# Performance work log

Hardware: AMD Instinct MI355X
Metric: run time of the kernel (lower is better)

Reference implementation:

```python
import jax, jax.numpy as jnp
import numpy as np

N = 100_000      # num nodes
E = 1_600_000    # num edges
F_IN = 128       # input feature dim
H = 128          # hidden dim
C = 16           # num classes
R = 5            # num relations


def setup_inputs() -> dict:
    key = jax.random.key(0)
    ks = jax.random.split(key, 12)
    x = jax.random.normal(ks[0], (N, F_IN), jnp.float32)
    edge_index = jax.random.randint(ks[1], (2, E), 0, N, dtype=jnp.int64)
    edge_weight = jax.random.uniform(ks[2], (E,), jnp.float32)
    edge_type = jax.random.randint(ks[3], (E,), 0, R, dtype=jnp.int64)
    # RGCNConv params (no basis decomposition): per-relation weight, root, bias
    s1 = 1.0 / np.sqrt(F_IN).astype(np.float32)
    s2 = 1.0 / np.sqrt(H).astype(np.float32)
    W1 = jax.random.normal(ks[4], (R, F_IN, H), jnp.float32) * s1
    root1 = jax.random.normal(ks[5], (F_IN, H), jnp.float32) * s1
    b1 = jnp.zeros((H,), jnp.float32)
    W2 = jax.random.normal(ks[6], (R, H, C), jnp.float32) * s2
    root2 = jax.random.normal(ks[7], (H, C), jnp.float32) * s2
    b2 = jnp.zeros((C,), jnp.float32)
    return {"x": x, "edge_index": edge_index, "edge_weight": edge_weight,
            "edge_type": edge_type, "W1": W1, "root1": root1, "b1": b1,
            "W2": W2, "root2": root2, "b2": b2}


def _rgcn_conv(x, src, dst, ew, et, W, root, b):
    """WeightedRGCNConv: per-relation weighted mean aggregation + relation matmul.

    Equivalent to the torch loop over relations: mask edges of type r,
    propagate with aggr='mean' (PyG RGCNConv default) on messages
    edge_weight * x[src], then h_r @ W[r], summed over r; plus root & bias.
    Vectorized by scattering into (dst, relation) buckets.
    """
    n, r = x.shape[0], W.shape[0]
    m = x[src] * ew[:, None]                       # [E, d_in] messages
    seg = dst * r + et                             # bucket = (dst node, relation)
    sums = jax.ops.segment_sum(m, seg, num_segments=n * r).reshape(n, r, -1)
    cnt = jax.ops.segment_sum(jnp.ones_like(ew), seg, num_segments=n * r)
    cnt = cnt.reshape(n, r, 1)
    agg = sums / jnp.maximum(cnt, 1.0)             # mean; 0 for empty buckets
    out = jnp.einsum('nri,rio->no', agg, W)        # sum_r H_r @ W_r
    return out + x @ root + b


def reference(x, edge_index, edge_weight, edge_type, W1, root1, b1, W2, root2, b2):
    src, dst = edge_index[0], edge_index[1]
    h = _rgcn_conv(x, src, dst, edge_weight, edge_type, W1, root1, b1)
    h = jax.nn.relu(h)  # dropout is identity in eval mode
    out = _rgcn_conv(h, src, dst, edge_weight, edge_type, W2, root2, b2)
    return jax.nn.log_softmax(out, axis=1)
```

## Files before the change

kernel.cpp:

```cpp
#include <hip/hip_runtime.h>

#define N_NODES 100000
#define N_EDGES 1600000
#define N_REL   5
#define NCOARSE  196
#define CAP      16384

using bf16x8 = __attribute__((ext_vector_type(8))) short;
using f32x4  = __attribute__((ext_vector_type(4))) float;
using f32x2  = __attribute__((ext_vector_type(2))) float;

__device__ __forceinline__ unsigned short f2bf(float f) {
    unsigned int u = __float_as_uint(f);
    u += 0x7fffu + ((u >> 16) & 1u);
    return (unsigned short)(u >> 16);
}
__device__ __forceinline__ float bfu(unsigned short u) { return __uint_as_float((unsigned int)u << 16); }

__global__ __launch_bounds__(1024) void partition_append(
    const int* __restrict__ src, const int* __restrict__ dstv,
    const float* __restrict__ ew, const int* __restrict__ et,
    int* __restrict__ ccur, int2* __restrict__ pe) {
    __shared__ int lh[256];
    __shared__ int lb[256];
    int tid = threadIdx.x;
    if (tid < 256) lh[tid] = 0;
    __syncthreads();
    int base = blockIdx.x * 4096;
    int key[4], rank[4], meta[4];
    float w[4];
    #pragma unroll
    for (int i = 0; i < 4; ++i) {
        int e = base + i * 1024 + tid;
        key[i] = -1;
        if (e < N_EDGES) {
            int d = dstv[e];
            key[i] = d >> 9;
            meta[i] = src[e] | (et[e] << 17) | ((d & 511) << 20);
            w[i] = ew[e];
            rank[i] = atomicAdd(&lh[key[i]], 1);
        }
    }
    __syncthreads();
    if (tid < 256) {
        int c = lh[tid];
        lb[tid] = c ? atomicAdd(&ccur[tid], c) : 0;
    }
    __syncthreads();
    #pragma unroll
    for (int i = 0; i < 4; ++i)
        if (key[i] >= 0) {
            int pos = lb[key[i]] + rank[i];
            if (pos < CAP)
                pe[((size_t)key[i] << 14) + pos] = make_int2(meta[i], __float_as_int(w[i]));
        }
}

__global__ __launch_bounds__(256) void cscan(const int* __restrict__ ccur,
                                             int* __restrict__ cstart) {
    __shared__ int lds[256];
    int tid = threadIdx.x;
    int v = ccur[tid];
    lds[tid] = v;
    __syncthreads();
    for (int d = 1; d < 256; d <<= 1) {
        int t = (tid >= d) ? lds[tid - d] : 0;
        __syncthreads();
        lds[tid] += t;
        __syncthreads();
    }
    cstart[tid] = lds[tid] - v;
}

__global__ __launch_bounds__(1024) void bucket_sort(
    const int* __restrict__ ccnt, const int* __restrict__ cstart,
    const int2* __restrict__ pe, int2* __restrict__ edges,
    int* __restrict__ nbase, int2* __restrict__ nbp) {
    int cb = blockIdx.x;
    int node0 = cb << 9;
    if (node0 >= N_NODES) return;
    int nNodes = N_NODES - node0; if (nNodes > 512) nNodes = 512;
    int nf = nNodes * N_REL;
    __shared__ int hist[2560];
    __shared__ int cur[2560];
    __shared__ int wtot[16];
    __shared__ int woff[16];
    int tid = threadIdx.x;
    int wid = tid >> 6, lane = tid & 63;
    int cnt = ccnt[cb]; if (cnt > CAP) cnt = CAP;
    int gbase = cstart[cb];
    const int2* my = pe + ((size_t)cb << 14);

    for (int i = tid; i < nf; i += 1024) hist[i] = 0;
    __syncthreads();
    for (int i = tid; i < cnt; i += 1024) {
        int m = my[i].x;
        atomicAdd(&hist[((m >> 20) & 511) * N_REL + ((m >> 17) & 7)], 1);
    }
    __syncthreads();

    int t0 = tid * 3;
    int a0 = (t0 + 0 < nf) ? hist[t0 + 0] : 0;
    int a1 = (t0 + 1 < nf) ? hist[t0 + 1] : 0;
    int a2 = (t0 + 2 < nf) ? hist[t0 + 2] : 0;
    int s = a0 + a1 + a2;
    int incl = s;
    #pragma unroll
    for (int d = 1; d < 64; d <<= 1) {
        int t = __shfl_up(incl, d);
        if (lane >= d) incl += t;
    }
    if (lane == 63) wtot[wid] = incl;
    __syncthreads();
    if (wid == 0 && lane < 16) {
        int v = wtot[lane];
        int inc2 = v;
        #pragma unroll
        for (int d = 1; d < 16; d <<= 1) {
            int t = __shfl_up(inc2, d);
            if (lane >= d) inc2 += t;
        }
        woff[lane] = inc2 - v;
    }
    __syncthreads();
    int excl = incl - s + woff[wid];
    if (t0 + 0 < nf) cur[t0 + 0] = excl;
    excl += a0;
    if (t0 + 1 < nf) cur[t0 + 1] = excl;
    excl += a1;
    if (t0 + 2 < nf) cur[t0 + 2] = excl;
    __syncthreads();

    for (int i = tid; i < nNodes; i += 1024) {
        int b = i * N_REL;
        int c0 = cur[b];
        int B1 = cur[b + 1] - c0, B2 = cur[b + 2] - c0;
        int B3 = cur[b + 3] - c0, B4 = cur[b + 4] - c0;
        int deg = cur[b + 4] + hist[b + 4] - c0;
        nbase[node0 + i] = gbase + c0;
        nbp[node0 + i] = make_int2(B1 | (B2 << 8) | (B3 << 16) | (B4 << 24), deg);
    }
    __syncthreads();

    for (int i = tid; i < cnt; i += 1024) {
        int2 r = my[i];
        int fb = ((r.x >> 20) & 511) * N_REL + ((r.x >> 17) & 7);
        int pos = gbase + atomicAdd(&cur[fb], 1);
        float wf = __int_as_float(r.y) / (float)hist[fb];
        edges[pos] = make_int2(r.x & 0xFFFFF, __float_as_int(wf));
    }
}

__global__ void cvt_feat(const float* __restrict__ x, ushort* __restrict__ xh,
                         unsigned int* __restrict__ xq) {
    int i = blockIdx.x * blockDim.x + threadIdx.x;
    if (i >= (N_NODES * 128) / 4) return;
    float4 v = reinterpret_cast<const float4*>(x)[i];
    ushort4 o;
    o.x = f2bf(v.x); o.y = f2bf(v.y); o.z = f2bf(v.z); o.w = f2bf(v.w);
    reinterpret_cast<ushort4*>(xh)[i] = o;
    int p = __builtin_amdgcn_cvt_pk_fp8_f32(v.x, v.y, 0, false);
    p = __builtin_amdgcn_cvt_pk_fp8_f32(v.z, v.w, p, true);
    xq[i] = (unsigned int)p;
}

__global__ void cvt_wstack(const float* __restrict__ W, const float* __restrict__ root,
                           ushort* __restrict__ Wt) {
    int t = blockIdx.x * blockDim.x + threadIdx.x;
    int o = blockIdx.y;
    int seg = t >> 7, k = t & 127;
    float v = (seg == 0) ? root[k * 128 + o] : W[(size_t)(seg - 1) * 128 * 128 + k * 128 + o];
    Wt[(size_t)o * 768 + t] = f2bf(v);
}

__global__ void cvt_w2(const float* __restrict__ W2, const float* __restrict__ root2,
                       ushort* __restrict__ Wt2s) {
    int i = blockIdx.x * blockDim.x + threadIdx.x;
    if (i >= 96 * 128) return;
    int o = i >> 7, k = i & 127;
    float v = (o < 16) ? root2[k * 16 + o]
                       : W2[((size_t)((o >> 4) - 1) * 128 + k) * 16 + (o & 15)];
    Wt2s[i] = f2bf(v);
}

__global__ __launch_bounds__(256) void gather_all(
    const ushort* __restrict__ featq,
    const int2* __restrict__ edges,
    const int* __restrict__ nbase,
    const int2* __restrict__ nbp,
    ushort* __restrict__ A,
    int node0) {
    int n = __builtin_amdgcn_readfirstlane(node0 + blockIdx.x * 4 + (threadIdx.x >> 6));
    int lane = threadIdx.x & 63;
    int o0  = __builtin_amdgcn_readfirstlane(nbase[n]);
    int bx  = __builtin_amdgcn_readfirstlane(nbp[n].x);
    int deg = __builtin_amdgcn_readfirstlane(nbp[n].y);
    unsigned int* Ap = reinterpret_cast<unsigned int*>(A) + (size_t)(n - node0) * 320;

    if (deg <= 64) {
        int2 er = (lane < deg) ? edges[o0 + lane] : make_int2(0, 0);
        unsigned long long bp = (unsigned long long)(unsigned)bx
                              | ((unsigned long long)(unsigned)deg << 32);
        float ax = 0.f, ay = 0.f;
        int seg = 0;
        auto flushAt = [&](int jj) {
            while (seg < 5 && jj == (int)((bp >> (seg * 8)) & 0xFFull)) {
                Ap[64 * seg + lane] =
                    (unsigned int)f2bf(ax) | ((unsigned int)f2bf(ay) << 16);
                ax = 0.f; ay = 0.f; ++seg;
            }
        };
        int deg8 = (deg + 7) & ~7;
        for (int j = 0; j < deg8; j += 8) {
            unsigned short q[8];
            float w[8];
            #pragma unroll
            for (int u = 0; u < 8; ++u) {
                int m = __builtin_amdgcn_readlane(er.x, j + u);
                q[u] = featq[((size_t)(m & 0x1FFFF) << 6) + lane];
            }
            #pragma unroll
            for (int u = 0; u < 8; ++u)
                w[u] = __uint_as_float(__builtin_amdgcn_readlane(er.y, j + u));
            #pragma unroll
            for (int u = 0; u < 8; ++u) {
                flushAt(j + u);
                f32x2 f = __builtin_amdgcn_cvt_pk_f32_fp8((int)q[u], false);
                ax = fmaf(w[u], f.x, ax); ay = fmaf(w[u], f.y, ay);
            }
        }
        while (seg < 5) {
            Ap[64 * seg + lane] =
                (unsigned int)f2bf(ax) | ((unsigned int)f2bf(ay) << 16);
            ax = 0.f; ay = 0.f; ++seg;
        }
    } else {
        int B[6];
        B[0] = 0; B[1] = bx & 0xFF; B[2] = (bx >> 8) & 0xFF;
        B[3] = (bx >> 16) & 0xFF; B[4] = (unsigned)bx >> 24; B[5] = deg;
        #pragma unroll
        for (int r = 0; r < 5; ++r) {
            int s0 = o0 + B[r], e1 = o0 + B[r + 1];
            float ax = 0.f, ay = 0.f;
            for (int base = s0; base < e1; base += 64) {
                int2 er = (base + lane < e1) ? edges[base + lane] : make_int2(0, 0);
                int m = e1 - base; if (m > 64) m = 64;
                for (int j = 0; j < m; ++j) {
                    int mm = __builtin_amdgcn_readlane(er.x, j);
                    float w = __uint_as_float(__builtin_amdgcn_readlane(er.y, j));
                    unsigned short qv = featq[((size_t)(mm & 0x1FFFF) << 6) + lane];
                    f32x2 f = __builtin_amdgcn_cvt_pk_f32_fp8((int)qv, false);
                    ax = fmaf(w, f.x, ax);
                    ay = fmaf(w, f.y, ay);
                }
            }
            Ap[r * 64 + lane] = (unsigned int)f2bf(ax) | ((unsigned int)f2bf(ay) << 16);
        }
    }
}

__global__ __launch_bounds__(256) void gemmL1f(
    const ushort* __restrict__ xh,
    const ushort* __restrict__ A,
    const ushort* __restrict__ Wt,
    const float* __restrict__ bias,
    const ushort* __restrict__ Wt2,
    ushort* __restrict__ Yh,
    int row0, int nrows) {
    __shared__ ushort lds[128 * 128];
    ushort* As = lds;
    ushort* Bs = lds + 128 * 64;
    const int tid = threadIdx.x, lane = tid & 63, wave = tid >> 6;
    const int m0 = blockIdx.x * 128;

    constexpr int MF = 4, NF = 4;
    const int wr0 = (wave >> 1) * 64;
    const int wc0 = (wave & 1) * 64;

    f32x4 acc[MF][NF] = {};

    for (int ks = 0; ks < 12; ++ks) {
        #pragma unroll
        for (int u = 0; u < 4; ++u) {
            int idx = tid + u * 256;
            int row = idx >> 3, slot = idx & 7;
            float4 v;
            if (ks < 2) {
                int gr = row0 + m0 + row; if (gr >= N_NODES) gr = N_NODES - 1;
                v = *reinterpret_cast<const float4*>(xh + (size_t)gr * 128 + ks * 64 + slot * 8);
            } else {
                v = *reinterpret_cast<const float4*>(
                    A + (size_t)(m0 + row) * 640 + (ks - 2) * 64 + slot * 8);
            }
            int byte = row * 128 + ((slot ^ (row & 7)) << 4);
            *reinterpret_cast<float4*>(reinterpret_cast<char*>(As) + byte) = v;
        }
        #pragma unroll
        for (int u = 0; u < 4; ++u) {
            int idx = tid + u * 256;
            int row = idx >> 3, slot = idx & 7;
            float4 v = *reinterpret_cast<const float4*>(
                Wt + (size_t)row * 768 + ks * 64 + slot * 8);
            int byte = row * 128 + ((slot ^ (row & 7)) << 4);
            *reinterpret_cast<float4*>(reinterpret_cast<char*>(Bs) + byte) = v;
        }
        __syncthreads();

        #pragma unroll
        for (int kh = 0; kh < 2; ++kh) {
            bf16x8 af[MF], bfr[NF];
            #pragma unroll
            for (int m = 0; m < MF; ++m) {
                int row = wr0 + m * 16 + (lane & 15);
                int slot = kh * 4 + (lane >> 4);
                int byte = row * 128 + ((slot ^ (row & 7)) << 4);
                af[m] = *reinterpret_cast<const bf16x8*>(
                    reinterpret_cast<const char*>(As) + byte);
            }
            #pragma unroll
            for (int nn = 0; nn < NF; ++nn) {
                int row = wc0 + nn * 16 + (lane & 15);
                int slot = kh * 4 + (lane >> 4);
                int byte = row * 128 + ((slot ^ (row & 7)) << 4);
                bfr[nn] = *reinterpret_cast<const bf16x8*>(
                    reinterpret_cast<const char*>(Bs) + byte);
            }
            #pragma unroll
            for (int m = 0; m < MF; ++m)
                #pragma unroll
                for (int nn = 0; nn < NF; ++nn)
                    acc[m][nn] = __builtin_amdgcn_mfma_f32_16x16x32_bf16(
                        af[m], bfr[nn], acc[m][nn], 0, 0, 0);
        }
        __syncthreads();
    }

    #pragma unroll
    for (int m = 0; m < MF; ++m) {
        int rloc = wr0 + m * 16 + (lane >> 4) * 4;
        #pragma unroll
        for (int nn = 0; nn < NF; ++nn) {
            int c = wc0 + nn * 16 + (lane & 15);
            float bv = bias[c];
            #pragma unroll
            for (int q = 0; q < 4; ++q) {
                int row = rloc + q;
                float v = fmaxf(acc[m][nn][q] + bv, 0.f);
                int byte = row * 256 + ((((c >> 3) ^ (row & 15)) << 4)) + (c & 7) * 2;
                *reinterpret_cast<ushort*>(reinterpret_cast<char*>(lds) + byte) = f2bf(v);
            }
        }
    }
    __syncthreads();

    f32x4 acc2[2][6] = {};
    #pragma unroll
    for (int ks = 0; ks < 4; ++ks) {
        bf16x8 af[2], bfr[6];
        #pragma unroll
        for (int m = 0; m < 2; ++m) {
            int row = wave * 32 + m * 16 + (lane & 15);
            int slot = ks * 4 + (lane >> 4);
            int byte = row * 256 + ((slot ^ (row & 15)) << 4);
            af[m] = *reinterpret_cast<const bf16x8*>(
                reinterpret_cast<const char*>(lds) + byte);
        }
        #pragma unroll
        for (int nn = 0; nn < 6; ++nn) {
            int row = nn * 16 + (lane & 15);
            int slot = ks * 4 + (lane >> 4);
            bfr[nn] = *reinterpret_cast<const bf16x8*>(
                Wt2 + (size_t)row * 128 + slot * 8);
        }
        #pragma unroll
        for (int m = 0; m < 2; ++m)
            #pragma unroll
            for (int nn = 0; nn < 6; ++nn)
                acc2[m][nn] = __builtin_amdgcn_mfma_f32_16x16x32_bf16(
                    af[m], bfr[nn], acc2[m][nn], 0, 0, 0);
    }

    #pragma unroll
    for (int m = 0; m < 2; ++m) {
        int rloc = wave * 32 + m * 16 + (lane >> 4) * 4;
        #pragma unroll
        for (int nn = 0; nn < 6; ++nn) {
            int c = nn * 16 + (lane & 15);
            #pragma unroll
            for (int q = 0; q < 4; ++q) {
                int lrow = m0 + rloc + q;
                int grow = row0 + lrow;
                if (lrow < nrows && grow < N_NODES)
                    Yh[(size_t)grow * 96 + c] = f2bf(acc2[m][nn][q]);
            }
        }
    }
}

__global__ __launch_bounds__(256) void agg2_softmax(
    const ushort* __restrict__ Yh, const int2* __restrict__ edges,
    const int* __restrict__ nbase, const int2* __restrict__ nbp,
    const float* __restrict__ b2, float* __restrict__ out) {
    int wave = threadIdx.x >> 6, lane = threadIdx.x & 63;
    int q = lane >> 4, c = lane & 15;
    int n = (blockIdx.x * 4 + wave) * 4 + q;
    int nn = (n < N_NODES) ? n : N_NODES - 1;
    int o0 = nbase[nn];
    int deg = nbp[nn].y;

    float val = bfu(Yh[(size_t)nn * 96 + c]) + b2[c];

    for (int b = 0; b < deg; b += 16) {
        int2 er = (b + c < deg) ? edges[o0 + b + c] : make_int2(0, 0);
        #pragma unroll
        for (int j = 0; j < 16; ++j) {
            int m = __shfl(er.x, q * 16 + j);
            float w = __uint_as_float(__shfl(er.y, q * 16 + j));
            int s = m & 0x1FFFF;
            int rel = (m >> 17) & 7;
            val = fmaf(w, bfu(Yh[(size_t)s * 96 + 16 + rel * 16 + c]), val);
        }
    }

    float mx = val;
    #pragma unroll
    for (int i = 1; i < 16; i <<= 1) mx = fmaxf(mx, __shfl_xor(mx, i));
    float ex = expf(val - mx);
    float ssum = ex;
    #pragma unroll
    for (int i = 1; i < 16; i <<= 1) ssum += __shfl_xor(ssum, i);
    float r = val - mx - logf(ssum);
    if (n < N_NODES) out[(size_t)n * 16 + c] = r;
}

extern "C" void kernel_launch(void* const* d_in, const int* in_sizes, int n_in,
                              void* d_out, int out_size, void* d_ws, size_t ws_size,
                              hipStream_t stream) {
    const float* x     = (const float*)d_in[0];
    const int*   ei    = (const int*)d_in[1];
    const int*   src   = ei;
    const int*   dst   = ei + N_EDGES;
    const float* ew    = (const float*)d_in[2];
    const int*   et    = (const int*)d_in[3];
    const float* W1    = (const float*)d_in[4];
    const float* root1 = (const float*)d_in[5];
    const float* b1    = (const float*)d_in[6];
    const float* W2    = (const float*)d_in[7];
    const float* root2 = (const float*)d_in[8];
    const float* b2    = (const float*)d_in[9];
    float* out = (float*)d_out;

    char* ws = (char*)d_ws;
    int*    ccur    = (int*)ws;
    int*    cstart  = (int*)(ws + 1024);
    int*    nbase   = (int*)(ws + 4096);
    int2*   nbp     = (int2*)(ws + 404096);
    int2*   edges   = (int2*)(ws + 1204096);
    ushort* xh      = (ushort*)(ws + 18018304);
    ushort* Wt1     = (ushort*)(ws + 43618304);
    ushort* Wt2s    = (ushort*)(ws + 43814912);
    unsigned int* xq = (unsigned int*)(ws + 43839488);
    int2*   pe      = (int2*)(ws + 56639488);
    ushort* Abuf    = (ushort*)(ws + 56639488);

    const int chunk = (ws_size >= 225000000ull) ? N_NODES : 25000;
    const int nch   = N_NODES / chunk;
    ushort* Yh = (ushort*)(ws + 56639488 +
        (chunk == N_NODES ? 128122880ull : 32112640ull));

    cvt_feat<<<((N_NODES * 128 / 4) + 255) / 256, 256, 0, stream>>>(x, xh, xq);
    cvt_wstack<<<dim3(3, 128), 256, 0, stream>>>(W1, root1, Wt1);
    cvt_w2<<<(96 * 128 + 255) / 256, 256, 0, stream>>>(W2, root2, Wt2s);

    hipMemsetAsync(ccur, 0, 1024, stream);
    partition_append<<<(N_EDGES + 4095) / 4096, 1024, 0, stream>>>(src, dst, ew, et, ccur, pe);
    cscan<<<1, 256, 0, stream>>>(ccur, cstart);
    bucket_sort<<<NCOARSE, 1024, 0, stream>>>(ccur, cstart, pe, edges, nbase, nbp);

    for (int cc = 0; cc < nch; ++cc) {
        gather_all<<<chunk / 4, 256, 0, stream>>>(
            (const ushort*)xq, edges, nbase, nbp, Abuf, cc * chunk);
        gemmL1f<<<(chunk + 127) / 128, 256, 0, stream>>>(
            xh, Abuf, Wt1, b1, Wt2s, Yh, cc * chunk, chunk);
    }

    agg2_softmax<<<(N_NODES + 15) / 16, 256, 0, stream>>>(
        Yh, edges, nbase, nbp, b2, out);
}
```

Measured before the change: 210.1 us.

## Transform-then-aggregate layer 1: precompute per-relation X·W_r in FP8, gather once

```diff
diff --git a/kernel.cpp b/kernel.cpp
--- a/kernel.cpp
+++ b/kernel.cpp
@@ -134,11 +134,9 @@
     for (int i = tid; i < nNodes; i += 1024) {
         int b = i * N_REL;
         int c0 = cur[b];
-        int B1 = cur[b + 1] - c0, B2 = cur[b + 2] - c0;
-        int B3 = cur[b + 3] - c0, B4 = cur[b + 4] - c0;
         int deg = cur[b + 4] + hist[b + 4] - c0;
         nbase[node0 + i] = gbase + c0;
-        nbp[node0 + i] = make_int2(B1 | (B2 << 8) | (B3 << 16) | (B4 << 24), deg);
+        nbp[node0 + i] = make_int2(0, deg);
     }
     __syncthreads();
 
@@ -151,26 +149,28 @@
     }
 }
 
-__global__ void cvt_feat(const float* __restrict__ x, ushort* __restrict__ xh,
-                         unsigned int* __restrict__ xq) {
+__global__ void cvt_feat(const float* __restrict__ x, ushort* __restrict__ xh) {
     int i = blockIdx.x * blockDim.x + threadIdx.x;
     if (i >= (N_NODES * 128) / 4) return;
     float4 v = reinterpret_cast<const float4*>(x)[i];
     ushort4 o;
     o.x = f2bf(v.x); o.y = f2bf(v.y); o.z = f2bf(v.z); o.w = f2bf(v.w);
     reinterpret_cast<ushort4*>(xh)[i] = o;
-    int p = __builtin_amdgcn_cvt_pk_fp8_f32(v.x, v.y, 0, false);
-    p = __builtin_amdgcn_cvt_pk_fp8_f32(v.z, v.w, p, true);
-    xq[i] = (unsigned int)p;
-}
-
-__global__ void cvt_wstack(const float* __restrict__ W, const float* __restrict__ root,
-                           ushort* __restrict__ Wt) {
-    int t = blockIdx.x * blockDim.x + threadIdx.x;
-    int o = blockIdx.y;
-    int seg = t >> 7, k = t & 127;
-    float v = (seg == 0) ? root[k * 128 + o] : W[(size_t)(seg - 1) * 128 * 128 + k * 128 + o];
-    Wt[(size_t)o * 768 + t] = f2bf(v);
+}
+
+__global__ void cvt_w1b(const float* __restrict__ W1, ushort* __restrict__ Wt1b) {
+    int i = blockIdx.x * blockDim.x + threadIdx.x;
+    if (i >= 640 * 128) return;
+    int o640 = i >> 7, k = i & 127;
+    int r = o640 >> 7, o = o640 & 127;
+    Wt1b[i] = f2bf(W1[((size_t)r * 128 + k) * 128 + o]);
+}
+
+__global__ void cvt_root(const float* __restrict__ root1, ushort* __restrict__ Wtroot) {
+    int i = blockIdx.x * blockDim.x + threadIdx.x;
+    if (i >= 128 * 128) return;
+    int o = i >> 7, k = i & 127;
+    Wtroot[i] = f2bf(root1[k * 128 + o]);
 }
 
 __global__ void cvt_w2(const float* __restrict__ W2, const float* __restrict__ root2,
@@ -183,33 +183,98 @@
     Wt2s[i] = f2bf(v);
 }
 
-__global__ __launch_bounds__(256) void gather_all(
-    const ushort* __restrict__ featq,
+__global__ __launch_bounds__(256) void gemmZ(
+    const ushort* __restrict__ xh, const ushort* __restrict__ Wt1b,
+    unsigned char* __restrict__ Zq) {
+    __shared__ ushort As[128 * 128];
+    __shared__ ushort Bs[128 * 128];
+    const int tid = threadIdx.x, lane = tid & 63, wave = tid >> 6;
+    const int m0 = blockIdx.x * 128;
+
+    #pragma unroll
+    for (int u = 0; u < 8; ++u) {
+        int idx = tid + u * 256;
+        int row = idx >> 4, slot = idx & 15;
+        int gr = m0 + row; if (gr >= N_NODES) gr = N_NODES - 1;
+        float4 v = *reinterpret_cast<const float4*>(xh + (size_t)gr * 128 + slot * 8);
+        int byte = row * 256 + ((slot ^ (row & 15)) << 4);
+        *reinterpret_cast<float4*>(reinterpret_cast<char*>(As) + byte) = v;
+    }
+
+    for (int seg = 0; seg < 5; ++seg) {
+        #pragma unroll
+        for (int u = 0; u < 8; ++u) {
+            int idx = tid + u * 256;
+            int row = idx >> 4, slot = idx & 15;
+            float4 v = *reinterpret_cast<const float4*>(
+                Wt1b + ((size_t)(seg * 128 + row)) * 128 + slot * 8);
+            int byte = row * 256 + ((slot ^ (row & 15)) << 4);
+            *reinterpret_cast<float4*>(reinterpret_cast<char*>(Bs) + byte) = v;
+        }
+        __syncthreads();
+
+        f32x4 acc[2][8] = {};
+        #pragma unroll
+        for (int ks = 0; ks < 4; ++ks) {
+            bf16x8 af[2], bfr[8];
+            #pragma unroll
+            for (int m = 0; m < 2; ++m) {
+                int row = wave * 32 + m * 16 + (lane & 15);
+                int slot = ks * 4 + (lane >> 4);
+                int byte = row * 256 + ((slot ^ (row & 15)) << 4);
+                af[m] = *reinterpret_cast<const bf16x8*>(
+                    reinterpret_cast<const char*>(As) + byte);
+            }
+            #pragma unroll
+            for (int nn = 0; nn < 8; ++nn) {
+                int row = nn * 16 + (lane & 15);
+                int slot = ks * 4 + (lane >> 4);
+                int byte = row * 256 + ((slot ^ (row & 15)) << 4);
+                bfr[nn] = *reinterpret_cast<const bf16x8*>(
+                    reinterpret_cast<const char*>(Bs) + byte);
+            }
+            #pragma unroll
+            for (int m = 0; m < 2; ++m)
+                #pragma unroll
+                for (int nn = 0; nn < 8; ++nn)
+                    acc[m][nn] = __builtin_amdgcn_mfma_f32_16x16x32_bf16(
+                        af[m], bfr[nn], acc[m][nn], 0, 0, 0);
+        }
+
+        #pragma unroll
+        for (int m = 0; m < 2; ++m) {
+            int rloc = m0 + wave * 32 + m * 16 + (lane >> 4) * 4;
+            #pragma unroll
+            for (int nn = 0; nn < 8; ++nn) {
+                int c = seg * 128 + nn * 16 + (lane & 15);
+                #pragma unroll
+                for (int q = 0; q < 4; ++q) {
+                    int row = rloc + q;
+                    if (row < N_NODES) {
+                        float v = acc[m][nn][q];
+                        int p = __builtin_amdgcn_cvt_pk_fp8_f32(v, v, 0, false);
+                        Zq[(size_t)row * 640 + c] = (unsigned char)(p & 0xFF);
+                    }
+                }
+            }
+        }
+        __syncthreads();
+    }
+}
+
+__global__ __launch_bounds__(256) void gather2(
+    const ushort* __restrict__ Zq,
     const int2* __restrict__ edges,
-    const int* __restrict__ nbase,
-    const int2* __restrict__ nbp,
-    ushort* __restrict__ A,
-    int node0) {
-    int n = __builtin_amdgcn_readfirstlane(node0 + blockIdx.x * 4 + (threadIdx.x >> 6));
+    const int* __restrict__ nbase, const int2* __restrict__ nbp,
+    ushort* __restrict__ hpre) {
+    int n = __builtin_amdgcn_readfirstlane(blockIdx.x * 4 + (threadIdx.x >> 6));
     int lane = threadIdx.x & 63;
     int o0  = __builtin_amdgcn_readfirstlane(nbase[n]);
-    int bx  = __builtin_amdgcn_readfirstlane(nbp[n].x);
     int deg = __builtin_amdgcn_readfirstlane(nbp[n].y);
-    unsigned int* Ap = reinterpret_cast<unsigned int*>(A) + (size_t)(n - node0) * 320;
+    float ax = 0.f, ay = 0.f;
 
     if (deg <= 64) {
         int2 er = (lane < deg) ? edges[o0 + lane] : make_int2(0, 0);
-        unsigned long long bp = (unsigned long long)(unsigned)bx
-                              | ((unsigned long long)(unsigned)deg << 32);
-        float ax = 0.f, ay = 0.f;
-        int seg = 0;
-        auto flushAt = [&](int jj) {
-            while (seg < 5 && jj == (int)((bp >> (seg * 8)) & 0xFFull)) {
-                Ap[64 * seg + lane] =
-                    (unsigned int)f2bf(ax) | ((unsigned int)f2bf(ay) << 16);
-                ax = 0.f; ay = 0.f; ++seg;
-            }
-        };
         int deg8 = (deg + 7) & ~7;
         for (int j = 0; j < deg8; j += 8) {
             unsigned short q[8];
@@ -217,153 +282,140 @@
             #pragma unroll
             for (int u = 0; u < 8; ++u) {
                 int m = __builtin_amdgcn_readlane(er.x, j + u);
-                q[u] = featq[((size_t)(m & 0x1FFFF) << 6) + lane];
+                int s5 = (m & 0x1FFFF) * 5 + ((m >> 17) & 7);
+                q[u] = Zq[((size_t)s5 << 6) + lane];
             }
             #pragma unroll
             for (int u = 0; u < 8; ++u)
                 w[u] = __uint_as_float(__builtin_amdgcn_readlane(er.y, j + u));
             #pragma unroll
             for (int u = 0; u < 8; ++u) {
-                flushAt(j + u);
                 f32x2 f = __builtin_amdgcn_cvt_pk_f32_fp8((int)q[u], false);
                 ax = fmaf(w[u], f.x, ax); ay = fmaf(w[u], f.y, ay);
             }
         }
-        while (seg < 5) {
-            Ap[64 * seg + lane] =
-                (unsigned int)f2bf(ax) | ((unsigned int)f2bf(ay) << 16);
-            ax = 0.f; ay = 0.f; ++seg;
-        }
     } else {
-        int B[6];
-        B[0] = 0; B[1] = bx & 0xFF; B[2] = (bx >> 8) & 0xFF;
-        B[3] = (bx >> 16) & 0xFF; B[4] = (unsigned)bx >> 24; B[5] = deg;
-        #pragma unroll
-        for (int r = 0; r < 5; ++r) {
-            int s0 = o0 + B[r], e1 = o0 + B[r + 1];
-            float ax = 0.f, ay = 0.f;
-            for (int base = s0; base < e1; base += 64) {
-                int2 er = (base + lane < e1) ? edges[base + lane] : make_int2(0, 0);
-                int m = e1 - base; if (m > 64) m = 64;
-                for (int j = 0; j < m; ++j) {
-                    int mm = __builtin_amdgcn_readlane(er.x, j);
-                    float w = __uint_as_float(__builtin_amdgcn_readlane(er.y, j));
-                    unsigned short qv = featq[((size_t)(mm & 0x1FFFF) << 6) + lane];
-                    f32x2 f = __builtin_amdgcn_cvt_pk_f32_fp8((int)qv, false);
-                    ax = fmaf(w, f.x, ax);
-                    ay = fmaf(w, f.y, ay);
+        for (int base = o0; base < o0 + deg; base += 64) {
+            int rem = o0 + deg - base;
+            int mcap = rem > 64 ? 64 : rem;
+            int2 er = (lane < mcap) ? edges[base + lane] : make_int2(0, 0);
+            int m8 = (mcap + 7) & ~7;
+            for (int j = 0; j < m8; j += 8) {
+                unsigned short q[8];
+                float w[8];
+                #pragma unroll
+                for (int u = 0; u < 8; ++u) {
+                    int m = __builtin_amdgcn_readlane(er.x, j + u);
+                    int s5 = (m & 0x1FFFF) * 5 + ((m >> 17) & 7);
+                    q[u] = Zq[((size_t)s5 << 6) + lane];
                 }
-            }
-            Ap[r * 64 + lane] = (unsigned int)f2bf(ax) | ((unsigned int)f2bf(ay) << 16);
-        }
-    }
-}
-
-__global__ __launch_bounds__(256) void gemmL1f(
+                #pragma unroll
+                for (int u = 0; u < 8; ++u)
+                    w[u] = __uint_as_float(__builtin_amdgcn_readlane(er.y, j + u));
+                #pragma unroll
+                for (int u = 0; u < 8; ++u) {
+                    f32x2 f = __builtin_amdgcn_cvt_pk_f32_fp8((int)q[u], false);
+                    ax = fmaf(w[u], f.x, ax); ay = fmaf(w[u], f.y, ay);
+                }
+            }
+        }
+    }
+
+    reinterpret_cast<unsigned int*>(hpre)[(size_t)n * 64 + lane] =
+        (unsigned int)f2bf(ax) | ((unsigned int)f2bf(ay) << 16);
+}
+
+__global__ __launch_bounds__(256) void gemmL1fr(
     const ushort* __restrict__ xh,
-    const ushort* __restrict__ A,
-    const ushort* __restrict__ Wt,
+    const ushort* __restrict__ Wtroot,
     const float* __restrict__ bias,
+    const ushort* __restrict__ hpre,
     const ushort* __restrict__ Wt2,
-    ushort* __restrict__ Yh,
-    int row0, int nrows) {
-    __shared__ ushort lds[128 * 128];
-    ushort* As = lds;
-    ushort* Bs = lds + 128 * 64;
+    ushort* __restrict__ Yh) {
+    __shared__ ushort As[128 * 128];
+    __shared__ ushort Bs[128 * 128];
     const int tid = threadIdx.x, lane = tid & 63, wave = tid >> 6;
     const int m0 = blockIdx.x * 128;
 
-    constexpr int MF = 4, NF = 4;
-    const int wr0 = (wave >> 1) * 64;
-    const int wc0 = (wave & 1) * 64;
-
-    f32x4 acc[MF][NF] = {};
-
-    for (int ks = 0; ks < 12; ++ks) {
-        #pragma unroll
-        for (int u = 0; u < 4; ++u) {
-            int idx = tid + u * 256;
-            int row = idx >> 3, slot = idx & 7;
-            float4 v;
-            if (ks < 2) {
-                int gr = row0 + m0 + row; if (gr >= N_NODES) gr = N_NODES - 1;
-                v = *reinterpret_cast<const float4*>(xh + (size_t)gr * 128 + ks * 64 + slot * 8);
-            } else {
-                v = *reinterpret_cast<const float4*>(
-                    A + (size_t)(m0 + row) * 640 + (ks - 2) * 64 + slot * 8);
-            }
-            int byte = row * 128 + ((slot ^ (row & 7)) << 4);
-            *reinterpret_cast<float4*>(reinterpret_cast<char*>(As) + byte) = v;
-        }
-        #pragma unroll
-        for (int u = 0; u < 4; ++u) {
-            int idx = tid + u * 256;
-            int row = idx >> 3, slot = idx & 7;
-            float4 v = *reinterpret_cast<const float4*>(
-                Wt + (size_t)row * 768 + ks * 64 + slot * 8);
-            int byte = row * 128 + ((slot ^ (row & 7)) << 4);
-            *reinterpret_cast<float4*>(reinterpret_cast<char*>(Bs) + byte) = v;
-        }
-        __syncthreads();
-
-        #pragma unroll
-        for (int kh = 0; kh < 2; ++kh) {
-            bf16x8 af[MF], bfr[NF];
-            #pragma unroll
-            for (int m = 0; m < MF; ++m) {
-                int row = wr0 + m * 16 + (lane & 15);
-                int slot = kh * 4 + (lane >> 4);
-                int byte = row * 128 + ((slot ^ (row & 7)) << 4);
-                af[m] = *reinterpret_cast<const bf16x8*>(
-                    reinterpret_cast<const char*>(As) + byte);
-            }
-            #pragma unroll
-            for (int nn = 0; nn < NF; ++nn) {
-                int row = wc0 + nn * 16 + (lane & 15);
-                int slot = kh * 4 + (lane >> 4);
-                int byte = row * 128 + ((slot ^ (row & 7)) << 4);
-                bfr[nn] = *reinterpret_cast<const bf16x8*>(
-                    reinterpret_cast<const char*>(Bs) + byte);
-            }
-            #pragma unroll
-            for (int m = 0; m < MF; ++m)
-                #pragma unroll
-                for (int nn = 0; nn < NF; ++nn)
-                    acc[m][nn] = __builtin_amdgcn_mfma_f32_16x16x32_bf16(
-                        af[m], bfr[nn], acc[m][nn], 0, 0, 0);
-        }
-        __syncthreads();
-    }
-
-    #pragma unroll
-    for (int m = 0; m < MF; ++m) {
-        int rloc = wr0 + m * 16 + (lane >> 4) * 4;
-        #pragma unroll
-        for (int nn = 0; nn < NF; ++nn) {
-            int c = wc0 + nn * 16 + (lane & 15);
-            float bv = bias[c];
-            #pragma unroll
-            for (int q = 0; q < 4; ++q) {
-                int row = rloc + q;
-                float v = fmaxf(acc[m][nn][q] + bv, 0.f);
-                int byte = row * 256 + ((((c >> 3) ^ (row & 15)) << 4)) + (c & 7) * 2;
-                *reinterpret_cast<ushort*>(reinterpret_cast<char*>(lds) + byte) = f2bf(v);
-            }
-        }
-    }
-    __syncthreads();
-
-    f32x4 acc2[2][6] = {};
+    #pragma unroll
+    for (int u = 0; u < 8; ++u) {
+        int idx = tid + u * 256;
+        int row = idx >> 4, slot = idx & 15;
+        int gr = m0 + row; if (gr >= N_NODES) gr = N_NODES - 1;
+        float4 v = *reinterpret_cast<const float4*>(xh + (size_t)gr * 128 + slot * 8);
+        int byte = row * 256 + ((slot ^ (row & 15)) << 4);
+        *reinterpret_cast<float4*>(reinterpret_cast<char*>(As) + byte) = v;
+    }
+    #pragma unroll
+    for (int u = 0; u < 8; ++u) {
+        int idx = tid + u * 256;
+        int row = idx >> 4, slot = idx & 15;
+        float4 v = *reinterpret_cast<const float4*>(Wtroot + (size_t)row * 128 + slot * 8);
+        int byte = row * 256 + ((slot ^ (row & 15)) << 4);
+        *reinterpret_cast<float4*>(reinterpret_cast<char*>(Bs) + byte) = v;
+    }
+    __syncthreads();
+
+    f32x4 acc[2][8] = {};
     #pragma unroll
     for (int ks = 0; ks < 4; ++ks) {
-        bf16x8 af[2], bfr[6];
+        bf16x8 af[2], bfr[8];
         #pragma unroll
         for (int m = 0; m < 2; ++m) {
             int row = wave * 32 + m * 16 + (lane & 15);
             int slot = ks * 4 + (lane >> 4);
             int byte = row * 256 + ((slot ^ (row & 15)) << 4);
             af[m] = *reinterpret_cast<const bf16x8*>(
-                reinterpret_cast<const char*>(lds) + byte);
+                reinterpret_cast<const char*>(As) + byte);
+        }
+        #pragma unroll
+        for (int nn = 0; nn < 8; ++nn) {
+            int row = nn * 16 + (lane & 15);
+            int slot = ks * 4 + (lane >> 4);
+            int byte = row * 256 + ((slot ^ (row & 15)) << 4);
+            bfr[nn] = *reinterpret_cast<const bf16x8*>(
+                reinterpret_cast<const char*>(Bs) + byte);
+        }
+        #pragma unroll
+        for (int m = 0; m < 2; ++m)
+            #pragma unroll
+            for (int nn = 0; nn < 8; ++nn)
+                acc[m][nn] = __builtin_amdgcn_mfma_f32_16x16x32_bf16(
+                    af[m], bfr[nn], acc[m][nn], 0, 0, 0);
+    }
+    __syncthreads();
+
+    #pragma unroll
+    for (int m = 0; m < 2; ++m) {
+        int rloc = wave * 32 + m * 16 + (lane >> 4) * 4;
+        #pragma unroll
+        for (int nn = 0; nn < 8; ++nn) {
+            int c = nn * 16 + (lane & 15);
+            float bv = bias[c];
+            #pragma unroll
+            for (int q = 0; q < 4; ++q) {
+                int row = rloc + q;
+                int grow = m0 + row; if (grow >= N_NODES) grow = N_NODES - 1;
+                float v = fmaxf(acc[m][nn][q] + bv +
+                                bfu(hpre[(size_t)grow * 128 + c]), 0.f);
+                int byte = row * 256 + ((((c >> 3) ^ (row & 15)) << 4)) + (c & 7) * 2;
+                *reinterpret_cast<ushort*>(reinterpret_cast<char*>(As) + byte) = f2bf(v);
+            }
+        }
+    }
+    __syncthreads();
+
+    f32x4 acc2[2][6] = {};
+    #pragma unroll
+    for (int ks = 0; ks < 4; ++ks) {
+        bf16x8 af[2], bfr[6];
+        #pragma unroll
+        for (int m = 0; m < 2; ++m) {
+            int row = wave * 32 + m * 16 + (lane & 15);
+            int slot = ks * 4 + (lane >> 4);
+            int byte = row * 256 + ((slot ^ (row & 15)) << 4);
+            af[m] = *reinterpret_cast<const bf16x8*>(
+                reinterpret_cast<const char*>(As) + byte);
         }
         #pragma unroll
         for (int nn = 0; nn < 6; ++nn) {
@@ -388,9 +440,8 @@
             int c = nn * 16 + (lane & 15);
             #pragma unroll
             for (int q = 0; q < 4; ++q) {
-                int lrow = m0 + rloc + q;
-                int grow = row0 + lrow;
-                if (lrow < nrows && grow < N_NODES)
+                int grow = m0 + rloc + q;
+                if (grow < N_NODES)
                     Yh[(size_t)grow * 96 + c] = f2bf(acc2[m][nn][q]);
             }
         }
@@ -456,20 +507,18 @@
     int*    nbase   = (int*)(ws + 4096);
     int2*   nbp     = (int2*)(ws + 404096);
     int2*   edges   = (int2*)(ws + 1204096);
-    ushort* xh      = (ushort*)(ws + 18018304);
-    ushort* Wt1     = (ushort*)(ws + 43618304);
-    ushort* Wt2s    = (ushort*)(ws + 43814912);
-    unsigned int* xq = (unsigned int*)(ws + 43839488);
-    int2*   pe      = (int2*)(ws + 56639488);
-    ushort* Abuf    = (ushort*)(ws + 56639488);
-
-    const int chunk = (ws_size >= 225000000ull) ? N_NODES : 25000;
-    const int nch   = N_NODES / chunk;
-    ushort* Yh = (ushort*)(ws + 56639488 +
-        (chunk == N_NODES ? 128122880ull : 32112640ull));
-
-    cvt_feat<<<((N_NODES * 128 / 4) + 255) / 256, 256, 0, stream>>>(x, xh, xq);
-    cvt_wstack<<<dim3(3, 128), 256, 0, stream>>>(W1, root1, Wt1);
+    ushort* xh      = (ushort*)(ws + 14004096);
+    ushort* Wt1b    = (ushort*)(ws + 39604096);
+    ushort* Wtroot  = (ushort*)(ws + 39767936);
+    ushort* Wt2s    = (ushort*)(ws + 39800704);
+    ushort* hpre    = (ushort*)(ws + 39825280);
+    unsigned char* Zq = (unsigned char*)(ws + 65425280);
+    ushort* Yh      = (ushort*)(ws + 129425280);
+    int2*   pe      = (int2*)(ws + 148625280);
+
+    cvt_feat<<<((N_NODES * 128 / 4) + 255) / 256, 256, 0, stream>>>(x, xh);
+    cvt_w1b<<<(640 * 128 + 255) / 256, 256, 0, stream>>>(W1, Wt1b);
+    cvt_root<<<(128 * 128 + 255) / 256, 256, 0, stream>>>(root1, Wtroot);
     cvt_w2<<<(96 * 128 + 255) / 256, 256, 0, stream>>>(W2, root2, Wt2s);
 
     hipMemsetAsync(ccur, 0, 1024, stream);
@@ -477,12 +526,13 @@
     cscan<<<1, 256, 0, stream>>>(ccur, cstart);
     bucket_sort<<<NCOARSE, 1024, 0, stream>>>(ccur, cstart, pe, edges, nbase, nbp);
 
-    for (int cc = 0; cc < nch; ++cc) {
-        gather_all<<<chunk / 4, 256, 0, stream>>>(
-            (const ushort*)xq, edges, nbase, nbp, Abuf, cc * chunk);
-        gemmL1f<<<(chunk + 127) / 128, 256, 0, stream>>>(
-            xh, Abuf, Wt1, b1, Wt2s, Yh, cc * chunk, chunk);
-    }
+    gemmZ<<<(N_NODES + 127) / 128, 256, 0, stream>>>(xh, Wt1b, Zq);
+
+    gather2<<<N_NODES / 4, 256, 0, stream>>>(
+        (const ushort*)Zq, edges, nbase, nbp, hpre);
+
+    gemmL1fr<<<(N_NODES + 127) / 128, 256, 0, stream>>>(
+        xh, Wtroot, b1, hpre, Wt2s, Yh);
 
     agg2_softmax<<<(N_NODES + 15) / 16, 256, 0, stream>>>(
         Yh, edges, nbase, nbp, b2, out);
```

New measurement: 205.8 us. 2.0% less time.
